# Performance work log

Measured on AMD Instinct MI355X. Metric: run time of the kernel, lower is better.

The kernel has to match this reference:

```python
import math
import jax, jax.numpy as jnp
import numpy as np

D_MODEL = 768
N_HEADS = 12


def setup_inputs() -> dict:
    key = jax.random.key(0)
    kx, kw, kb = jax.random.split(key, 3)
    x = jax.random.normal(kx, (2, 2048, D_MODEL), dtype=jnp.float32)
    # nn.Linear(D, 3D): weight [3D, D], bias [3D]; init ~ U(-1/sqrt(D), 1/sqrt(D))
    bound = 1.0 / math.sqrt(D_MODEL)
    W_kqv = jax.random.uniform(kw, (3 * D_MODEL, D_MODEL), dtype=jnp.float32, minval=-bound, maxval=bound)
    b_kqv = jax.random.uniform(kb, (3 * D_MODEL,), dtype=jnp.float32, minval=-bound, maxval=bound)
    return {"x": x, "W_kqv": W_kqv, "b_kqv": b_kqv}


def reference(x, W_kqv, b_kqv):
    N, C, D = x.shape
    H = N_HEADS
    hd = D // H
    z = jnp.einsum('ncd,ed->nce', x, W_kqv) + b_kqv  # [N, C, 3D]
    # order in source: k first, then q, then v
    k = z[:, :, :D].reshape(N, C, H, hd).transpose(0, 2, 1, 3)       # [N,H,C,hd]
    q = z[:, :, D:2 * D].reshape(N, C, H, hd).transpose(0, 2, 1, 3)
    v = z[:, :, 2 * D:].reshape(N, C, H, hd).transpose(0, 2, 1, 3)
    # NOTE: faithful to source: scale by sqrt(D) (full model dim), not sqrt(head_dim)
    scores = jnp.einsum('nhqd,nhkd->nhqk', q, k) / math.sqrt(D)
    causal = jnp.tril(jnp.ones((C, C), dtype=bool))
    scores = jnp.where(causal, scores, -jnp.inf)
    attn = jax.nn.softmax(scores, axis=-1)
    out = jnp.einsum('nhqk,nhkd->nhqd', attn, v)  # [N,H,C,hd]
    return out.transpose(0, 2, 1, 3).reshape(N, C, D)
```

## Files before the change

kernel.cpp:

```cpp
#include <hip/hip_runtime.h>
#include <stdint.h>

#define D_MODEL 768
#define E3      2304
#define NCTX    2048
#define NH      12
#define HD      64
#define MROWS   4096
#define NHTOT   24

typedef __attribute__((ext_vector_type(8))) short short8;
typedef __attribute__((ext_vector_type(4))) short bf16x4;
typedef __attribute__((ext_vector_type(4))) float f32x4;

typedef __attribute__((address_space(3))) uint32_t lds_u32;
typedef __attribute__((address_space(1))) uint32_t glob_u32;

__device__ __forceinline__ void async_copy16(const void* g, void* l) {
    __builtin_amdgcn_global_load_lds((const glob_u32*)(uintptr_t)g,
                                     (lds_u32*)(uint32_t)(uintptr_t)l, 16, 0, 0);
}

__device__ __forceinline__ unsigned short f2bf(float f) {
    uint32_t u = __builtin_bit_cast(uint32_t, f);
    u += 0x7fffu + ((u >> 16) & 1u);
    return (unsigned short)(u >> 16);
}

__device__ __forceinline__ float fast_exp2(float x) {
#if __has_builtin(__builtin_amdgcn_exp2f)
    return __builtin_amdgcn_exp2f(x);
#else
    return __expf(x * 0.6931471805599453f);
#endif
}

#if __has_builtin(__builtin_amdgcn_mfma_f32_16x16x16bf16_1k)
#define HAVE_MFMA16 1
#else
#define HAVE_MFMA16 0
#endif

__global__ __launch_bounds__(256) void cast2_bf16_kernel(const float* __restrict__ a,
                                                         unsigned short* __restrict__ oa,
                                                         int na4,
                                                         const float* __restrict__ b,
                                                         unsigned short* __restrict__ ob) {
    int i = blockIdx.x * blockDim.x + threadIdx.x;
    const float4* src;
    ushort4* dst;
    int idx;
    if (i < na4) { src = (const float4*)a; dst = (ushort4*)oa; idx = i; }
    else         { src = (const float4*)b; dst = (ushort4*)ob; idx = i - na4; }
    float4 v = src[idx];
    ushort4 o;
    o.x = f2bf(v.x); o.y = f2bf(v.y); o.z = f2bf(v.z); o.w = f2bf(v.w);
    dst[idx] = o;
}

__global__ __launch_bounds__(256) void qkv_gemm(const unsigned short* __restrict__ A,
                                                const unsigned short* __restrict__ B,
                                                const float* __restrict__ bias,
                                                unsigned short* __restrict__ Zq,
                                                unsigned short* __restrict__ Kb,
                                                unsigned short* __restrict__ Vb) {
    __shared__ __attribute__((aligned(16))) unsigned short sA[128 * 64];
    __shared__ __attribute__((aligned(16))) unsigned short sB[128 * 64];

    const int tid  = threadIdx.x;
    const int wave = tid >> 6;
    const int lane = tid & 63;
    const int quad = lane >> 4;
    const int l15  = lane & 15;
    const int wm   = (wave >> 1) << 6;
    const int wn   = (wave & 1) << 6;
    const int row0 = blockIdx.y * 128;
    const int col0 = blockIdx.x * 128;

    const int srow   = lane >> 3;
    const int schunk = (lane & 7) * 8;

    f32x4 acc[4][4] = {};

    for (int k0 = 0; k0 < D_MODEL; k0 += 64) {
        __syncthreads();
#pragma unroll
        for (int c = 0; c < 4; ++c) {
            const int rbase = wave * 32 + c * 8;
            async_copy16(A + (size_t)(row0 + rbase + srow) * D_MODEL + k0 + schunk, &sA[rbase * 64]);
            async_copy16(B + (size_t)(col0 + rbase + srow) * D_MODEL + k0 + schunk, &sB[rbase * 64]);
        }
        __syncthreads();

#pragma unroll
        for (int ks = 0; ks < 2; ++ks) {
            short8 aF[4], bF[4];
#pragma unroll
            for (int i = 0; i < 4; ++i)
                aF[i] = *(const short8*)&sA[(wm + i * 16 + l15) * 64 + ks * 32 + quad * 8];
#pragma unroll
            for (int i = 0; i < 4; ++i)
                bF[i] = *(const short8*)&sB[(wn + i * 16 + l15) * 64 + ks * 32 + quad * 8];
#pragma unroll
            for (int i = 0; i < 4; ++i)
#pragma unroll
                for (int j = 0; j < 4; ++j)
                    acc[i][j] = __builtin_amdgcn_mfma_f32_16x16x32_bf16(aF[i], bF[j], acc[i][j], 0, 0, 0);
        }
    }

    if (col0 < D_MODEL) {
#pragma unroll
        for (int j = 0; j < 4; ++j) {
            const int col = col0 + wn + j * 16 + l15;
            const float bv = bias[col];
            const int h = col >> 6, d = col & 63;
            const int ks = d >> 5, quadd = (d >> 3) & 3, e = d & 7;
#pragma unroll
            for (int i = 0; i < 4; ++i) {
                const int row = row0 + wm + i * 16 + quad * 4;
                const int n = row >> 11;
                const int key = row & (NCTX - 1);
                const int kb = key >> 6;
                const int ct = i;
                const size_t base = ((size_t)((n * NH + h) * 32 + kb)) * 4096
                                  + (((ks * 4 + ct) * 4 + quadd) * 16) * 8 + e;
#pragma unroll
                for (int r = 0; r < 4; ++r)
                    Kb[base + (size_t)(quad * 4 + r) * 8] = f2bf(acc[i][j][r] + bv);
            }
        }
    } else if (col0 < 2 * D_MODEL) {
        const float zscale = 0.036084391824351615f * 1.4426950408889634f;
#pragma unroll
        for (int j = 0; j < 4; ++j) {
            const int col = col0 - D_MODEL + wn + j * 16 + l15;
            const float bv = bias[col0 + wn + j * 16 + l15];
#pragma unroll
            for (int i = 0; i < 4; ++i) {
                const int row = row0 + wm + i * 16 + quad * 4;
#pragma unroll
                for (int r = 0; r < 4; ++r)
                    Zq[(size_t)(row + r) * D_MODEL + col] = f2bf((acc[i][j][r] + bv) * zscale);
            }
        }
    } else {
#pragma unroll
        for (int j = 0; j < 4; ++j) {
            const int col = col0 + wn + j * 16 + l15;
            const float bv = bias[col];
            const int ch = col - 2 * D_MODEL;
            const int h = ch >> 6, d = ch & 63;
            const int dt = d >> 4, l15d = d & 15;
#pragma unroll
            for (int i = 0; i < 4; ++i) {
                const int row = row0 + wm + i * 16 + quad * 4;
                const int n = row >> 11;
                const int key = row & (NCTX - 1);
                const int kb = key >> 6;
                const int ct = i, quadv = quad;
                ushort4 w4;
                w4.x = f2bf(acc[i][j][0] + bv);
                w4.y = f2bf(acc[i][j][1] + bv);
                w4.z = f2bf(acc[i][j][2] + bv);
                w4.w = f2bf(acc[i][j][3] + bv);
                *(ushort4*)&Vb[((size_t)((n * NH + h) * 32 + kb)) * 4096
                               + (((ct * 4 + dt) * 4 + quadv) * 16 + l15d) * 4] = w4;
            }
        }
    }
}

__global__ __launch_bounds__(512) void attn_kernel(const unsigned short* __restrict__ Zq,
                                                   const unsigned short* __restrict__ Kb,
                                                   const unsigned short* __restrict__ Vb,
                                                   float* __restrict__ out) {
    __shared__ __attribute__((aligned(16))) unsigned short sK[2][2][4096];
    __shared__ __attribute__((aligned(16))) unsigned short sV[2][2][4096];
#if !HAVE_MFMA16
    __shared__ __attribute__((aligned(16))) unsigned short sP[8][16 * 72];
#endif

    const int tid  = threadIdx.x;
    const int wave = tid >> 6;
    const int half = wave >> 2;
    const int wv   = wave & 3;
    const int lane = tid & 63;
    const int quad = lane >> 4;
    const int l15  = lane & 15;
    const int b    = blockIdx.x;
    const int xcd  = b & 7;
    const int ii   = b >> 3;
    const int t    = 31 - ii / 3;
    const int nh   = (ii % 3) * 8 + xcd;
    const int n    = nh / NH;
    const int h    = nh - n * NH;

    const int nA    = (t + 2) >> 1;
    const int nB    = t + 1 - nA;
    const int kbase = half ? nA : 0;
    const int nMy   = half ? nB : nA;

    const unsigned short* KbP = Kb + (size_t)(nh * 32) * 4096;
    const unsigned short* VbP = Vb + (size_t)(nh * 32) * 4096;

    const unsigned short* Qp = Zq + (size_t)(n * NCTX + t * 64 + wv * 16) * D_MODEL + h * HD;
    short8 qf[2];
#pragma unroll
    for (int ks = 0; ks < 2; ++ks)
        qf[ks] = *(const short8*)&Qp[(size_t)l15 * D_MODEL + ks * 32 + quad * 8];

    f32x4 o[4] = {};
    float lsum = 0.0f;

#define STAGE(kbi, bufi)                                                          \
    do {                                                                          \
        const size_t gof = (size_t)(kbi) * 4096;                                  \
        _Pragma("unroll")                                                         \
        for (int c = 0; c < 2; ++c) {                                             \
            const int off = wv * 1024 + c * 512;                                  \
            async_copy16(KbP + gof + off + lane * 8, &sK[half][bufi][off]);       \
            async_copy16(VbP + gof + off + lane * 8, &sV[half][bufi][off]);       \
        }                                                                         \
    } while (0)

    if (nMy > 0) STAGE(kbase, 0);

    for (int i = 0; i < nA; ++i) {
        __syncthreads();
        if (i + 1 < nMy) STAGE(kbase + i + 1, (i + 1) & 1);

        if (i < nMy) {
            const int kb  = kbase + i;
            const int buf = i & 1;

            short8 kf[2][4];
#pragma unroll
            for (int ks = 0; ks < 2; ++ks)
#pragma unroll
                for (int ct = 0; ct < 4; ++ct)
                    kf[ks][ct] = *(const short8*)&sK[half][buf][(ks * 4 + ct) * 512 + lane * 8];

            f32x4 s[4] = {};
#pragma unroll
            for (int ct = 0; ct < 4; ++ct) {
                s[ct] = __builtin_amdgcn_mfma_f32_16x16x32_bf16(kf[0][ct], qf[0], s[ct], 0, 0, 0);
                s[ct] = __builtin_amdgcn_mfma_f32_16x16x32_bf16(kf[1][ct], qf[1], s[ct], 0, 0, 0);
            }

            const bool diag = (kb == t);
            const int qg = t * 64 + wv * 16 + l15;
#if HAVE_MFMA16
            bf16x4 pA[4];
#endif
#pragma unroll
            for (int ct = 0; ct < 4; ++ct) {
                float pv[4];
#pragma unroll
                for (int r = 0; r < 4; ++r) {
                    const int key = kb * 64 + ct * 16 + quad * 4 + r;
                    float sv = s[ct][r];
                    if (diag && key > qg) sv = -INFINITY;
                    pv[r] = fast_exp2(sv);
                    lsum += pv[r];
                }
#if HAVE_MFMA16
                pA[ct][0] = (short)f2bf(pv[0]); pA[ct][1] = (short)f2bf(pv[1]);
                pA[ct][2] = (short)f2bf(pv[2]); pA[ct][3] = (short)f2bf(pv[3]);
#else
                ushort4 w4;
                w4.x = f2bf(pv[0]); w4.y = f2bf(pv[1]); w4.z = f2bf(pv[2]); w4.w = f2bf(pv[3]);
                *(ushort4*)&sP[wave][l15 * 72 + ct * 16 + quad * 4] = w4;
#endif
            }

#if HAVE_MFMA16
#pragma unroll
            for (int ct = 0; ct < 4; ++ct)
#pragma unroll
                for (int dt = 0; dt < 4; ++dt) {
                    const bf16x4 vf = *(const bf16x4*)&sV[half][buf][(ct * 4 + dt) * 256 + lane * 4];
                    o[dt] = __builtin_amdgcn_mfma_f32_16x16x16bf16_1k(pA[ct], vf, o[dt], 0, 0, 0);
                }
#else
            const short8 pf0 = *(const short8*)&sP[wave][l15 * 72 + quad * 8];
            const short8 pf1 = *(const short8*)&sP[wave][l15 * 72 + 32 + quad * 8];
#pragma unroll
            for (int dt = 0; dt < 4; ++dt) {
                short8 vf0, vf1;
#pragma unroll
                for (int e = 0; e < 8; ++e) {
                    const int k0 = quad * 8 + e;
                    const int k1 = 32 + quad * 8 + e;
                    vf0[e] = (short)sV[half][buf][(((k0 >> 4) * 4 + dt) * 4 + ((k0 >> 2) & 3)) * 64 + l15 * 4 + (k0 & 3)];
                    vf1[e] = (short)sV[half][buf][(((k1 >> 4) * 4 + dt) * 4 + ((k1 >> 2) & 3)) * 64 + l15 * 4 + (k1 & 3)];
                }
                o[dt] = __builtin_amdgcn_mfma_f32_16x16x32_bf16(pf0, vf0, o[dt], 0, 0, 0);
                o[dt] = __builtin_amdgcn_mfma_f32_16x16x32_bf16(pf1, vf1, o[dt], 0, 0, 0);
            }
#endif
        }
    }
#undef STAGE

    float l = lsum;
    l += __shfl_xor(l, 16);
    l += __shfl_xor(l, 32);

    __syncthreads();
    float* red = (float*)&sK[0][0][0];
    if (half == 1) {
        float* po = red + wv * 1040;
#pragma unroll
        for (int dt = 0; dt < 4; ++dt)
#pragma unroll
            for (int r = 0; r < 4; ++r)
                po[(quad * 4 + r) * 64 + dt * 16 + l15] = o[dt][r];
        if (quad == 0) po[1024 + l15] = l;
    }
    __syncthreads();
    if (half == 0) {
        const float* po = red + wv * 1040;
        const float l2 = po[1024 + l15];
        const float linv = 1.0f / (l + l2);
#pragma unroll
        for (int r = 0; r < 4; ++r) {
            const float inv = __shfl(linv, quad * 4 + r);
            const size_t row = (size_t)n * NCTX + t * 64 + wv * 16 + quad * 4 + r;
#pragma unroll
            for (int dt = 0; dt < 4; ++dt)
                out[row * D_MODEL + h * HD + dt * 16 + l15] =
                    (o[dt][r] + po[(quad * 4 + r) * 64 + dt * 16 + l15]) * inv;
        }
    }
}

extern "C" void kernel_launch(void* const* d_in, const int* in_sizes, int n_in,
                              void* d_out, int out_size, void* d_ws, size_t ws_size,
                              hipStream_t stream) {
    const float* x = (const float*)d_in[0];
    const float* W = (const float*)d_in[1];
    const float* b = (const float*)d_in[2];
    float* out = (float*)d_out;

    unsigned short* xb = (unsigned short*)d_ws;
    unsigned short* Wb = xb + (size_t)MROWS * D_MODEL;
    unsigned short* Zq = Wb + (size_t)E3 * D_MODEL;
    unsigned short* Kb = Zq + (size_t)MROWS * D_MODEL;
    unsigned short* Vb = Kb + (size_t)NHTOT * 32 * 4096;

    const int NA4 = MROWS * D_MODEL / 4;
    const int NW4 = E3 * D_MODEL / 4;
    cast2_bf16_kernel<<<dim3((NA4 + NW4) / 256), 256, 0, stream>>>(x, xb, NA4, W, Wb);
    qkv_gemm<<<dim3(E3 / 128, MROWS / 128), 256, 0, stream>>>(xb, Wb, b, Zq, Kb, Vb);
    attn_kernel<<<dim3(NHTOT * (NCTX / 64)), 512, 0, stream>>>(Zq, Kb, Vb, out);
}
```

Baseline: 140.5 us.

## Split attention work per wave into 32 queries by half the key block

Each wave now handles 32 query rows against half of each 64-key block instead of 16 query rows against the whole block. K and V fragments loaded from LDS are reused across two query groups, which cuts LDS read traffic per MFMA. The price is a four-way cross-wave reduction of partial outputs and row sums through shared memory at the end. The launch bounds also gain a minimum-occupancy hint of 4.

After: 141.8 us. About the same (+0.9%).

```diff
diff --git a/kernel.cpp b/kernel.cpp
--- a/kernel.cpp
+++ b/kernel.cpp
@@ -171,12 +171,12 @@
     }
 }
 
-__global__ __launch_bounds__(512) void attn_kernel(const unsigned short* __restrict__ Zq,
-                                                   const unsigned short* __restrict__ Kb,
-                                                   const unsigned short* __restrict__ Vb,
-                                                   float* __restrict__ out) {
-    __shared__ __attribute__((aligned(16))) unsigned short sK[2][2][4096];
-    __shared__ __attribute__((aligned(16))) unsigned short sV[2][2][4096];
+__global__ __launch_bounds__(512, 4) void attn_kernel(const unsigned short* __restrict__ Zq,
+                                                      const unsigned short* __restrict__ Kb,
+                                                      const unsigned short* __restrict__ Vb,
+                                                      float* __restrict__ out) {
+    __shared__ __attribute__((aligned(16))) unsigned short sM[2][2][2][4096];
+    __shared__ float Lred[2][4][32];
 #if !HAVE_MFMA16
     __shared__ __attribute__((aligned(16))) unsigned short sP[8][16 * 72];
 #endif
@@ -184,7 +184,9 @@
     const int tid  = threadIdx.x;
     const int wave = tid >> 6;
     const int half = wave >> 2;
-    const int wv   = wave & 3;
+    const int w03  = wave & 3;
+    const int cw   = w03 & 1;
+    const int qw   = w03 >> 1;
     const int lane = tid & 63;
     const int quad = lane >> 4;
     const int l15  = lane & 15;
@@ -204,24 +206,26 @@
     const unsigned short* KbP = Kb + (size_t)(nh * 32) * 4096;
     const unsigned short* VbP = Vb + (size_t)(nh * 32) * 4096;
 
-    const unsigned short* Qp = Zq + (size_t)(n * NCTX + t * 64 + wv * 16) * D_MODEL + h * HD;
-    short8 qf[2];
-#pragma unroll
-    for (int ks = 0; ks < 2; ++ks)
-        qf[ks] = *(const short8*)&Qp[(size_t)l15 * D_MODEL + ks * 32 + quad * 8];
-
-    f32x4 o[4] = {};
-    float lsum = 0.0f;
-
-#define STAGE(kbi, bufi)                                                          \
-    do {                                                                          \
-        const size_t gof = (size_t)(kbi) * 4096;                                  \
-        _Pragma("unroll")                                                         \
-        for (int c = 0; c < 2; ++c) {                                             \
-            const int off = wv * 1024 + c * 512;                                  \
-            async_copy16(KbP + gof + off + lane * 8, &sK[half][bufi][off]);       \
-            async_copy16(VbP + gof + off + lane * 8, &sV[half][bufi][off]);       \
-        }                                                                         \
+    const unsigned short* Qp = Zq + (size_t)(n * NCTX + t * 64 + qw * 32) * D_MODEL + h * HD;
+    short8 qf[2][2];
+#pragma unroll
+    for (int g2 = 0; g2 < 2; ++g2)
+#pragma unroll
+        for (int ks = 0; ks < 2; ++ks)
+            qf[g2][ks] = *(const short8*)&Qp[(size_t)(g2 * 16 + l15) * D_MODEL + ks * 32 + quad * 8];
+
+    f32x4 o[2][4] = {};
+    float lsum[2] = {0.0f, 0.0f};
+
+#define STAGE(kbi, bufi)                                                            \
+    do {                                                                            \
+        const size_t gof = (size_t)(kbi) * 4096;                                    \
+        _Pragma("unroll")                                                           \
+        for (int c = 0; c < 2; ++c) {                                               \
+            const int off = w03 * 1024 + c * 512;                                   \
+            async_copy16(KbP + gof + off + lane * 8, &sM[0][half][bufi][off]);      \
+            async_copy16(VbP + gof + off + lane * 8, &sM[1][half][bufi][off]);      \
+        }                                                                           \
     } while (0)
 
     if (nMy > 0) STAGE(kbase, 0);
@@ -234,104 +238,126 @@
             const int kb  = kbase + i;
             const int buf = i & 1;
 
-            short8 kf[2][4];
+            short8 kf[2][2];
 #pragma unroll
             for (int ks = 0; ks < 2; ++ks)
 #pragma unroll
-                for (int ct = 0; ct < 4; ++ct)
-                    kf[ks][ct] = *(const short8*)&sK[half][buf][(ks * 4 + ct) * 512 + lane * 8];
-
-            f32x4 s[4] = {};
-#pragma unroll
-            for (int ct = 0; ct < 4; ++ct) {
-                s[ct] = __builtin_amdgcn_mfma_f32_16x16x32_bf16(kf[0][ct], qf[0], s[ct], 0, 0, 0);
-                s[ct] = __builtin_amdgcn_mfma_f32_16x16x32_bf16(kf[1][ct], qf[1], s[ct], 0, 0, 0);
-            }
+                for (int c2 = 0; c2 < 2; ++c2)
+                    kf[ks][c2] = *(const short8*)&sM[0][half][buf][(ks * 4 + (cw * 2 + c2)) * 512 + lane * 8];
+
+#if HAVE_MFMA16
+            bf16x4 vf[2][4];
+#pragma unroll
+            for (int c2 = 0; c2 < 2; ++c2)
+#pragma unroll
+                for (int dt = 0; dt < 4; ++dt)
+                    vf[c2][dt] = *(const bf16x4*)&sM[1][half][buf][((cw * 2 + c2) * 4 + dt) * 256 + lane * 4];
+#endif
 
             const bool diag = (kb == t);
-            const int qg = t * 64 + wv * 16 + l15;
+#pragma unroll
+            for (int g2 = 0; g2 < 2; ++g2) {
+                f32x4 s[2] = {};
+#pragma unroll
+                for (int c2 = 0; c2 < 2; ++c2) {
+                    s[c2] = __builtin_amdgcn_mfma_f32_16x16x32_bf16(kf[0][c2], qf[g2][0], s[c2], 0, 0, 0);
+                    s[c2] = __builtin_amdgcn_mfma_f32_16x16x32_bf16(kf[1][c2], qf[g2][1], s[c2], 0, 0, 0);
+                }
+
+                const int qg = t * 64 + qw * 32 + g2 * 16 + l15;
 #if HAVE_MFMA16
-            bf16x4 pA[4];
-#endif
-#pragma unroll
-            for (int ct = 0; ct < 4; ++ct) {
-                float pv[4];
-#pragma unroll
-                for (int r = 0; r < 4; ++r) {
-                    const int key = kb * 64 + ct * 16 + quad * 4 + r;
-                    float sv = s[ct][r];
-                    if (diag && key > qg) sv = -INFINITY;
-                    pv[r] = fast_exp2(sv);
-                    lsum += pv[r];
+                bf16x4 pA[2];
+#endif
+#pragma unroll
+                for (int c2 = 0; c2 < 2; ++c2) {
+                    float pv[4];
+#pragma unroll
+                    for (int r = 0; r < 4; ++r) {
+                        const int key = kb * 64 + (cw * 2 + c2) * 16 + quad * 4 + r;
+                        float sv = s[c2][r];
+                        if (diag && key > qg) sv = -INFINITY;
+                        pv[r] = fast_exp2(sv);
+                        lsum[g2] += pv[r];
+                    }
+#if HAVE_MFMA16
+                    pA[c2][0] = (short)f2bf(pv[0]); pA[c2][1] = (short)f2bf(pv[1]);
+                    pA[c2][2] = (short)f2bf(pv[2]); pA[c2][3] = (short)f2bf(pv[3]);
+#else
+                    ushort4 w4;
+                    w4.x = f2bf(pv[0]); w4.y = f2bf(pv[1]); w4.z = f2bf(pv[2]); w4.w = f2bf(pv[3]);
+                    *(ushort4*)&sP[wave][l15 * 72 + c2 * 16 + quad * 4] = w4;
+#endif
                 }
+
 #if HAVE_MFMA16
-                pA[ct][0] = (short)f2bf(pv[0]); pA[ct][1] = (short)f2bf(pv[1]);
-                pA[ct][2] = (short)f2bf(pv[2]); pA[ct][3] = (short)f2bf(pv[3]);
+#pragma unroll
+                for (int c2 = 0; c2 < 2; ++c2)
+#pragma unroll
+                    for (int dt = 0; dt < 4; ++dt)
+                        o[g2][dt] = __builtin_amdgcn_mfma_f32_16x16x16bf16_1k(pA[c2], vf[c2][dt], o[g2][dt], 0, 0, 0);
 #else
-                ushort4 w4;
-                w4.x = f2bf(pv[0]); w4.y = f2bf(pv[1]); w4.z = f2bf(pv[2]); w4.w = f2bf(pv[3]);
-                *(ushort4*)&sP[wave][l15 * 72 + ct * 16 + quad * 4] = w4;
-#endif
-            }
-
-#if HAVE_MFMA16
-#pragma unroll
-            for (int ct = 0; ct < 4; ++ct)
+                const short8 pf = *(const short8*)&sP[wave][l15 * 72 + quad * 8];
 #pragma unroll
                 for (int dt = 0; dt < 4; ++dt) {
-                    const bf16x4 vf = *(const bf16x4*)&sV[half][buf][(ct * 4 + dt) * 256 + lane * 4];
-                    o[dt] = __builtin_amdgcn_mfma_f32_16x16x16bf16_1k(pA[ct], vf, o[dt], 0, 0, 0);
+                    short8 vf0;
+#pragma unroll
+                    for (int e = 0; e < 8; ++e) {
+                        const int k0 = quad * 8 + e;
+                        const int ct = cw * 2 + (k0 >> 4), qv = (k0 >> 2) & 3, e2 = k0 & 3;
+                        vf0[e] = (short)sM[1][half][buf][(ct * 4 + dt) * 256 + qv * 64 + l15 * 4 + e2];
+                    }
+                    o[g2][dt] = __builtin_amdgcn_mfma_f32_16x16x32_bf16(pf, vf0, o[g2][dt], 0, 0, 0);
                 }
-#else
-            const short8 pf0 = *(const short8*)&sP[wave][l15 * 72 + quad * 8];
-            const short8 pf1 = *(const short8*)&sP[wave][l15 * 72 + 32 + quad * 8];
-#pragma unroll
-            for (int dt = 0; dt < 4; ++dt) {
-                short8 vf0, vf1;
-#pragma unroll
-                for (int e = 0; e < 8; ++e) {
-                    const int k0 = quad * 8 + e;
-                    const int k1 = 32 + quad * 8 + e;
-                    vf0[e] = (short)sV[half][buf][(((k0 >> 4) * 4 + dt) * 4 + ((k0 >> 2) & 3)) * 64 + l15 * 4 + (k0 & 3)];
-                    vf1[e] = (short)sV[half][buf][(((k1 >> 4) * 4 + dt) * 4 + ((k1 >> 2) & 3)) * 64 + l15 * 4 + (k1 & 3)];
-                }
-                o[dt] = __builtin_amdgcn_mfma_f32_16x16x32_bf16(pf0, vf0, o[dt], 0, 0, 0);
-                o[dt] = __builtin_amdgcn_mfma_f32_16x16x32_bf16(pf1, vf1, o[dt], 0, 0, 0);
-            }
-#endif
+#endif
+            }
         }
     }
 #undef STAGE
 
-    float l = lsum;
-    l += __shfl_xor(l, 16);
-    l += __shfl_xor(l, 32);
+    float lr[2];
+#pragma unroll
+    for (int g2 = 0; g2 < 2; ++g2) {
+        float l = lsum[g2];
+        l += __shfl_xor(l, 16);
+        l += __shfl_xor(l, 32);
+        lr[g2] = l;
+    }
 
     __syncthreads();
-    float* red = (float*)&sK[0][0][0];
-    if (half == 1) {
-        float* po = red + wv * 1040;
-#pragma unroll
-        for (int dt = 0; dt < 4; ++dt)
-#pragma unroll
-            for (int r = 0; r < 4; ++r)
-                po[(quad * 4 + r) * 64 + dt * 16 + l15] = o[dt][r];
-        if (quad == 0) po[1024 + l15] = l;
+    float* R = (float*)&sM[0][0][0][0];
+    const int hc = half * 2 + cw;
+    {
+        float* po = R + (size_t)(qw * 4 + hc) * 2048;
+#pragma unroll
+        for (int g2 = 0; g2 < 2; ++g2) {
+#pragma unroll
+            for (int dt = 0; dt < 4; ++dt)
+#pragma unroll
+                for (int rr = 0; rr < 4; ++rr)
+                    po[(g2 * 16 + quad * 4 + rr) * 64 + dt * 16 + l15] = o[g2][dt][rr];
+            if (quad == 0) Lred[qw][hc][g2 * 16 + l15] = lr[g2];
+        }
     }
     __syncthreads();
     if (half == 0) {
-        const float* po = red + wv * 1040;
-        const float l2 = po[1024 + l15];
-        const float linv = 1.0f / (l + l2);
-#pragma unroll
-        for (int r = 0; r < 4; ++r) {
-            const float inv = __shfl(linv, quad * 4 + r);
-            const size_t row = (size_t)n * NCTX + t * 64 + wv * 16 + quad * 4 + r;
-#pragma unroll
-            for (int dt = 0; dt < 4; ++dt)
-                out[row * D_MODEL + h * HD + dt * 16 + l15] =
-                    (o[dt][r] + po[(quad * 4 + r) * 64 + dt * 16 + l15]) * inv;
-        }
+        const float* Rq = R + (size_t)qw * 4 * 2048;
+#pragma unroll
+        for (int g2 = 0; g2 < 2; ++g2)
+#pragma unroll
+            for (int rr = 0; rr < 4; ++rr) {
+                const int qr = g2 * 16 + quad * 4 + rr;
+                const float ls = Lred[qw][0][qr] + Lred[qw][1][qr] + Lred[qw][2][qr] + Lred[qw][3][qr];
+                const float inv = 1.0f / ls;
+                const size_t row = (size_t)n * NCTX + t * 64 + qw * 32 + qr;
+#pragma unroll
+                for (int dtl = 0; dtl < 2; ++dtl) {
+                    const int dt = cw * 2 + dtl;
+                    const int col = dt * 16 + l15;
+                    const float v = Rq[0 * 2048 + qr * 64 + col] + Rq[1 * 2048 + qr * 64 + col]
+                                  + Rq[2 * 2048 + qr * 64 + col] + Rq[3 * 2048 + qr * 64 + col];
+                    out[row * D_MODEL + h * HD + col] = v * inv;
+                }
+            }
     }
 }
 
```
